# Optimization experiments

Hardware: AMD Instinct MI355X
Metric: run time of the kernel (lower is better)

Reference implementation:

```python
import jax, jax.numpy as jnp
import numpy as np

B, N = 2, 2000
C_IN, RH, RW = 256, 7, 7
D_FLAT = C_IN * RH * RW  # 12544
D_OUT = 1024
NUM_CLASSES = 10


def setup_inputs() -> dict:
    key = jax.random.key(0)
    ks = jax.random.split(key, 10)
    s1 = 1.0 / np.sqrt(D_FLAT)
    s2 = 1.0 / np.sqrt(D_OUT)
    return {
        "features": jax.random.normal(ks[0], (B, N, C_IN, RH, RW), jnp.float32),
        "boxes": jax.random.normal(ks[1], (B, N, 5), jnp.float32),
        "w1": jax.random.uniform(ks[2], (D_FLAT, D_OUT), jnp.float32, -s1, s1),
        "b1": jax.random.uniform(ks[3], (D_OUT,), jnp.float32, -s1, s1),
        "w2": jax.random.uniform(ks[4], (D_OUT, D_OUT), jnp.float32, -s2, s2),
        "b2": jax.random.uniform(ks[5], (D_OUT,), jnp.float32, -s2, s2),
        "wc": jax.random.uniform(ks[6], (D_OUT, NUM_CLASSES + 1), jnp.float32, -s2, s2),
        "bc": jax.random.uniform(ks[7], (NUM_CLASSES + 1,), jnp.float32, -s2, s2),
        "wr": jax.random.uniform(ks[8], (D_OUT, 5), jnp.float32, -s2, s2),
        "br": jax.random.uniform(ks[9], (5,), jnp.float32, -s2, s2),
    }


def reference(features, boxes, w1, b1, w2, b2, wc, bc, wr, br):
    # Flatten(start_dim=2): [B, N, C*7*7]
    x = features.reshape(B, N, D_FLAT)
    # fc: Linear -> ReLU -> Linear -> ReLU
    h = jax.nn.relu(jnp.einsum("bnd,de->bne", x, w1) + b1)
    h = jax.nn.relu(jnp.einsum("bnd,de->bne", h, w2) + b2)
    classification = jnp.einsum("bnd,dc->bnc", h, wc) + bc  # [B, N, num_classes+1]
    regression = jnp.einsum("bnd,dr->bnr", h, wr) + br      # [B, N, 5]
    boxes_out = boxes + regression
    rois = boxes
    return classification, boxes_out, rois
```

## Files before the change

kernel.cpp:

```cpp
#include <hip/hip_runtime.h>
#include <stdint.h>

#define GAS __attribute__((address_space(1)))
#define LAS __attribute__((address_space(3)))

typedef short bf16x8 __attribute__((ext_vector_type(8)));
typedef float f32x4 __attribute__((ext_vector_type(4)));
typedef unsigned short u16x8 __attribute__((ext_vector_type(8)));

__device__ __forceinline__ unsigned short f2bf(float f) {
  union { float f; uint32_t u; } v; v.f = f;
  uint32_t r = v.u + 0x7FFFu + ((v.u >> 16) & 1u);
  return (unsigned short)(r >> 16);
}

__global__ __launch_bounds__(256) void cvt_kernel(const float* __restrict__ src,
                                                  unsigned short* __restrict__ dst,
                                                  long n8) {
  long i = (long)blockIdx.x * blockDim.x + threadIdx.x;
  if (i >= n8) return;
  const float4* s4 = (const float4*)src;
  float4 a = s4[i * 2];
  float4 b = s4[i * 2 + 1];
  u16x8 o;
  o[0] = f2bf(a.x); o[1] = f2bf(a.y); o[2] = f2bf(a.z); o[3] = f2bf(a.w);
  o[4] = f2bf(b.x); o[5] = f2bf(b.y); o[6] = f2bf(b.z); o[7] = f2bf(b.w);
  ((u16x8*)dst)[i] = o;
}

__global__ __launch_bounds__(256) void transpose_cvt(const float* __restrict__ src,
                                                     unsigned short* __restrict__ dst,
                                                     int R, int C) {
  __shared__ unsigned short tile[32][33];
  int tx = threadIdx.x, ty = threadIdx.y;
  int r0 = blockIdx.y * 32, c0 = blockIdx.x * 32;
#pragma unroll
  for (int i = 0; i < 32; i += 8)
    tile[ty + i][tx] = f2bf(src[(long)(r0 + ty + i) * C + c0 + tx]);
  __syncthreads();
#pragma unroll
  for (int i = 0; i < 32; i += 8)
    dst[(long)(c0 + ty + i) * R + r0 + tx] = tile[tx][ty + i];
}

__global__ __launch_bounds__(256) void bias_relu_cvt(const float* __restrict__ acc,
                                                     const float* __restrict__ bias,
                                                     unsigned short* __restrict__ dst) {
  long i = (long)blockIdx.x * 256 + threadIdx.x;
  const float4* a4 = (const float4*)acc;
  float4 a = a4[i * 2];
  float4 b = a4[i * 2 + 1];
  int col = (int)((i * 8) & 1023);
  const float4* b4 = (const float4*)(bias + col);
  float4 ba = b4[0], bb = b4[1];
  u16x8 o;
  o[0] = f2bf(fmaxf(a.x + ba.x, 0.f)); o[1] = f2bf(fmaxf(a.y + ba.y, 0.f));
  o[2] = f2bf(fmaxf(a.z + ba.z, 0.f)); o[3] = f2bf(fmaxf(a.w + ba.w, 0.f));
  o[4] = f2bf(fmaxf(b.x + bb.x, 0.f)); o[5] = f2bf(fmaxf(b.y + bb.y, 0.f));
  o[6] = f2bf(fmaxf(b.z + bb.z, 0.f)); o[7] = f2bf(fmaxf(b.w + bb.w, 0.f));
  ((u16x8*)dst)[i] = o;
}

template <int ATOMIC, int STORE_BF16>
__global__ __launch_bounds__(256, 2) void gemm_bt(const unsigned short* __restrict__ A,
                                                  const unsigned short* __restrict__ Bt,
                                                  const float* __restrict__ bias,
                                                  void* __restrict__ Cv, int M, int K,
                                                  int kIters) {
  __shared__ unsigned short lA[128 * 64];
  __shared__ unsigned short lB[128 * 64];
  const int tid = threadIdx.x;
  const int lane = tid & 63;
  const int wave = tid >> 6;
  const int wm = wave >> 1, wn = wave & 1;
  const long rowBase = (long)blockIdx.y * 128;
  const long colBase = (long)blockIdx.x * 128;
  const int kStart = blockIdx.z * kIters * 64;

  f32x4 acc[4][4];
#pragma unroll
  for (int i = 0; i < 4; i++)
#pragma unroll
    for (int j = 0; j < 4; j++) acc[i][j] = (f32x4){0.f, 0.f, 0.f, 0.f};

  long gA[4], gB[4];
#pragma unroll
  for (int it = 0; it < 4; ++it) {
    int f = it * 256 + tid;
    int r = f >> 3;
    int q = f & 7;
    int kq = ((q ^ (r & 7)) * 8) + kStart;
    long ar = rowBase + r;
    if (ar >= M) ar = M - 1;
    gA[it] = ar * (long)K + kq;
    gB[it] = (colBase + r) * (long)K + kq;
  }

  for (int ki = 0; ki < kIters; ++ki) {
    const long kc = (long)ki * 64;
#pragma unroll
    for (int it = 0; it < 4; ++it) {
      int f = it * 256 + tid;
      __builtin_amdgcn_global_load_lds((const GAS void*)(A + gA[it] + kc),
                                       (LAS void*)(lA + f * 8), 16, 0, 0);
    }
#pragma unroll
    for (int it = 0; it < 4; ++it) {
      int f = it * 256 + tid;
      __builtin_amdgcn_global_load_lds((const GAS void*)(Bt + gB[it] + kc),
                                       (LAS void*)(lB + f * 8), 16, 0, 0);
    }
    __syncthreads();
#pragma unroll
    for (int ks = 0; ks < 64; ks += 32) {
      bf16x8 af[4], bf[4];
      const int c = (ks >> 3) + (lane >> 4);
      const int slot = (c ^ (lane & 7)) << 3;
      const int mr = wm * 64 + (lane & 15);
      const int nr = wn * 64 + (lane & 15);
#pragma unroll
      for (int i = 0; i < 4; i++)
        af[i] = *(const bf16x8*)(lA + (mr + i * 16) * 64 + slot);
#pragma unroll
      for (int i = 0; i < 4; i++)
        bf[i] = *(const bf16x8*)(lB + (nr + i * 16) * 64 + slot);
#pragma unroll
      for (int i = 0; i < 4; i++)
#pragma unroll
        for (int j = 0; j < 4; j++)
          acc[i][j] = __builtin_amdgcn_mfma_f32_16x16x32_bf16(af[i], bf[j], acc[i][j], 0, 0, 0);
    }
    __syncthreads();
  }

  const int cq = lane & 15;
  const int rq = (lane >> 4) * 4;
#pragma unroll
  for (int i = 0; i < 4; i++) {
#pragma unroll
    for (int j = 0; j < 4; j++) {
      int col = (int)colBase + wn * 64 + j * 16 + cq;
      float bv = ATOMIC ? 0.f : bias[col];
#pragma unroll
      for (int r = 0; r < 4; r++) {
        long grow = rowBase + wm * 64 + i * 16 + rq + r;
        if (grow < M) {
          if (ATOMIC) {
            unsafeAtomicAdd(&((float*)Cv)[grow * 1024 + col], acc[i][j][r]);
          } else {
            float v = acc[i][j][r] + bv;
            v = v > 0.f ? v : 0.f;
            if (STORE_BF16)
              ((unsigned short*)Cv)[grow * 1024 + col] = f2bf(v);
            else
              ((float*)Cv)[grow * 1024 + col] = v;
          }
        }
      }
    }
  }
}

__global__ __launch_bounds__(256) void head_kernel(
    const float* __restrict__ H2, const float* __restrict__ wc, const float* __restrict__ bc,
    const float* __restrict__ wr, const float* __restrict__ br, const float* __restrict__ boxes,
    float* __restrict__ cls, float* __restrict__ bout, float* __restrict__ rois) {
  const int lane = threadIdx.x & 63;
  const int wave = threadIdx.x >> 6;
  const int row = blockIdx.x * 4 + wave;
  const float* h = H2 + (long)row * 1024;
  float acc[16];
#pragma unroll
  for (int c = 0; c < 16; c++) acc[c] = 0.f;
#pragma unroll
  for (int i = 0; i < 16; i++) {
    int d = i * 64 + lane;
    float hv = h[d];
#pragma unroll
    for (int c = 0; c < 11; c++) acc[c] += hv * wc[d * 11 + c];
#pragma unroll
    for (int c = 0; c < 5; c++) acc[11 + c] += hv * wr[d * 5 + c];
  }
#pragma unroll
  for (int off = 32; off >= 1; off >>= 1) {
#pragma unroll
    for (int c = 0; c < 16; c++) acc[c] += __shfl_down(acc[c], off);
  }
  if (lane == 0) {
#pragma unroll
    for (int c = 0; c < 11; c++) cls[row * 11 + c] = acc[c] + bc[c];
#pragma unroll
    for (int c = 0; c < 5; c++) {
      float rg = acc[11 + c] + br[c];
      float bx = boxes[row * 5 + c];
      bout[row * 5 + c] = bx + rg;
      rois[row * 5 + c] = bx;
    }
  }
}

extern "C" void kernel_launch(void* const* d_in, const int* in_sizes, int n_in,
                              void* d_out, int out_size, void* d_ws, size_t ws_size,
                              hipStream_t stream) {
  const float* features = (const float*)d_in[0];
  const float* boxes = (const float*)d_in[1];
  const float* w1 = (const float*)d_in[2];
  const float* b1 = (const float*)d_in[3];
  const float* w2 = (const float*)d_in[4];
  const float* b2 = (const float*)d_in[5];
  const float* wc = (const float*)d_in[6];
  const float* bc = (const float*)d_in[7];
  const float* wr = (const float*)d_in[8];
  const float* br = (const float*)d_in[9];

  char* ws = (char*)d_ws;
  unsigned short* Xb  = (unsigned short*)ws;
  unsigned short* W1T = (unsigned short*)(ws + 100352000);
  unsigned short* W2T = (unsigned short*)(ws + 126042112);
  unsigned short* H1  = (unsigned short*)(ws + 128139264);
  float*          H2  = (float*)(ws + 136331264);
  float*          H1f = H2;

  hipMemsetAsync(H1f, 0, 16384000, stream);
  {
    long n8 = 50176000 / 8;
    cvt_kernel<<<(int)(n8 / 256), 256, 0, stream>>>(features, Xb, n8);
  }
  transpose_cvt<<<dim3(32, 392), dim3(32, 8), 0, stream>>>(w1, W1T, 12544, 1024);
  transpose_cvt<<<dim3(32, 32), dim3(32, 8), 0, stream>>>(w2, W2T, 1024, 1024);
  gemm_bt<1, 0><<<dim3(8, 32, 4), 256, 0, stream>>>(Xb, W1T, b1, H1f, 4000, 12544, 49);
  bias_relu_cvt<<<2000, 256, 0, stream>>>(H1f, b1, H1);
  gemm_bt<0, 0><<<dim3(8, 32, 1), 256, 0, stream>>>(H1, W2T, b2, H2, 4000, 1024, 16);
  float* cls = (float*)d_out;
  float* bout = cls + 44000;
  float* rois = cls + 64000;
  head_kernel<<<1000, 256, 0, stream>>>(H2, wc, bc, wr, br, boxes, cls, bout, rois);
}
```

Before: 546.5 us.

## Fuse fp32-to-bf16 conversion into GEMM1 A-load, split-K GEMM2, XCD-aware block mapping

Removes the separate feature conversion pass: GEMM1 now reads fp32 features directly, truncates them to bf16 with byte-permutes, and writes them to LDS, which drops a full read/write pass over the 200MB input. GEMM2 becomes split-K with atomic accumulation across 4 partitions, with bias and ReLU moved into the head kernel. Blocks are launched on a 1D grid remapped so that neighbouring tiles share an XCD for L2 reuse. The costs are register-staged loads in place of direct-to-LDS loads, truncation instead of round-to-nearest for the features, a larger memset, and extra atomics in GEMM2.

```diff
diff --git a/kernel.cpp b/kernel.cpp
--- a/kernel.cpp
+++ b/kernel.cpp
@@ -12,20 +12,6 @@
   union { float f; uint32_t u; } v; v.f = f;
   uint32_t r = v.u + 0x7FFFu + ((v.u >> 16) & 1u);
   return (unsigned short)(r >> 16);
-}
-
-__global__ __launch_bounds__(256) void cvt_kernel(const float* __restrict__ src,
-                                                  unsigned short* __restrict__ dst,
-                                                  long n8) {
-  long i = (long)blockIdx.x * blockDim.x + threadIdx.x;
-  if (i >= n8) return;
-  const float4* s4 = (const float4*)src;
-  float4 a = s4[i * 2];
-  float4 b = s4[i * 2 + 1];
-  u16x8 o;
-  o[0] = f2bf(a.x); o[1] = f2bf(a.y); o[2] = f2bf(a.z); o[3] = f2bf(a.w);
-  o[4] = f2bf(b.x); o[5] = f2bf(b.y); o[6] = f2bf(b.z); o[7] = f2bf(b.w);
-  ((u16x8*)dst)[i] = o;
 }
 
 __global__ __launch_bounds__(256) void transpose_cvt(const float* __restrict__ src,
@@ -61,11 +47,10 @@
   ((u16x8*)dst)[i] = o;
 }
 
-template <int ATOMIC, int STORE_BF16>
-__global__ __launch_bounds__(256, 2) void gemm_bt(const unsigned short* __restrict__ A,
+template <int A_FP32>
+__global__ __launch_bounds__(256, 2) void gemm_bt(const void* __restrict__ Av,
                                                   const unsigned short* __restrict__ Bt,
-                                                  const float* __restrict__ bias,
-                                                  void* __restrict__ Cv, int M, int K,
+                                                  float* __restrict__ Cv, int M, int K,
                                                   int kIters) {
   __shared__ unsigned short lA[128 * 64];
   __shared__ unsigned short lB[128 * 64];
@@ -73,9 +58,18 @@
   const int lane = tid & 63;
   const int wave = tid >> 6;
   const int wm = wave >> 1, wn = wave & 1;
-  const long rowBase = (long)blockIdx.y * 128;
-  const long colBase = (long)blockIdx.x * 128;
-  const int kStart = blockIdx.z * kIters * 64;
+
+  const int b = blockIdx.x;
+  const int xcd = b & 7;
+  const int slot = b >> 3;
+  const int bx = slot & 7;
+  const int pg = xcd * 16 + (slot >> 3);
+  const int by = pg & 31;
+  const int bz = pg >> 5;
+
+  const long rowBase = (long)by * 128;
+  const long colBase = (long)bx * 128;
+  const int kStart = bz * kIters * 64;
 
   f32x4 acc[4][4];
 #pragma unroll
@@ -93,16 +87,39 @@
     long ar = rowBase + r;
     if (ar >= M) ar = M - 1;
     gA[it] = ar * (long)K + kq;
-    gB[it] = (colBase + r) * (long)K + kq;
+    gB[it] = ((long)(colBase + r)) * K + kq;
   }
 
   for (int ki = 0; ki < kIters; ++ki) {
     const long kc = (long)ki * 64;
-#pragma unroll
-    for (int it = 0; it < 4; ++it) {
-      int f = it * 256 + tid;
-      __builtin_amdgcn_global_load_lds((const GAS void*)(A + gA[it] + kc),
-                                       (LAS void*)(lA + f * 8), 16, 0, 0);
+    if (A_FP32) {
+      const uint4* A4 = (const uint4*)Av;
+      uint4 t[8];
+#pragma unroll
+      for (int it = 0; it < 4; ++it) {
+        long fi = (gA[it] + kc) >> 2;
+        t[2 * it] = A4[fi];
+        t[2 * it + 1] = A4[fi + 1];
+      }
+#pragma unroll
+      for (int it = 0; it < 4; ++it) {
+        int f = it * 256 + tid;
+        uint4 lo = t[2 * it], hi = t[2 * it + 1];
+        uint4 o;
+        o.x = __builtin_amdgcn_perm(lo.y, lo.x, 0x07060302u);
+        o.y = __builtin_amdgcn_perm(lo.w, lo.z, 0x07060302u);
+        o.z = __builtin_amdgcn_perm(hi.y, hi.x, 0x07060302u);
+        o.w = __builtin_amdgcn_perm(hi.w, hi.z, 0x07060302u);
+        *(uint4*)(lA + f * 8) = o;
+      }
+    } else {
+      const unsigned short* A = (const unsigned short*)Av;
+#pragma unroll
+      for (int it = 0; it < 4; ++it) {
+        int f = it * 256 + tid;
+        __builtin_amdgcn_global_load_lds((const GAS void*)(A + gA[it] + kc),
+                                         (LAS void*)(lA + f * 8), 16, 0, 0);
+      }
     }
 #pragma unroll
     for (int it = 0; it < 4; ++it) {
@@ -115,15 +132,15 @@
     for (int ks = 0; ks < 64; ks += 32) {
       bf16x8 af[4], bf[4];
       const int c = (ks >> 3) + (lane >> 4);
-      const int slot = (c ^ (lane & 7)) << 3;
+      const int slotk = (c ^ (lane & 7)) << 3;
       const int mr = wm * 64 + (lane & 15);
       const int nr = wn * 64 + (lane & 15);
 #pragma unroll
       for (int i = 0; i < 4; i++)
-        af[i] = *(const bf16x8*)(lA + (mr + i * 16) * 64 + slot);
+        af[i] = *(const bf16x8*)(lA + (mr + i * 16) * 64 + slotk);
 #pragma unroll
       for (int i = 0; i < 4; i++)
-        bf[i] = *(const bf16x8*)(lB + (nr + i * 16) * 64 + slot);
+        bf[i] = *(const bf16x8*)(lB + (nr + i * 16) * 64 + slotk);
 #pragma unroll
       for (int i = 0; i < 4; i++)
 #pragma unroll
@@ -140,42 +157,32 @@
 #pragma unroll
     for (int j = 0; j < 4; j++) {
       int col = (int)colBase + wn * 64 + j * 16 + cq;
-      float bv = ATOMIC ? 0.f : bias[col];
 #pragma unroll
       for (int r = 0; r < 4; r++) {
         long grow = rowBase + wm * 64 + i * 16 + rq + r;
-        if (grow < M) {
-          if (ATOMIC) {
-            unsafeAtomicAdd(&((float*)Cv)[grow * 1024 + col], acc[i][j][r]);
-          } else {
-            float v = acc[i][j][r] + bv;
-            v = v > 0.f ? v : 0.f;
-            if (STORE_BF16)
-              ((unsigned short*)Cv)[grow * 1024 + col] = f2bf(v);
-            else
-              ((float*)Cv)[grow * 1024 + col] = v;
-          }
-        }
+        if (grow < M) unsafeAtomicAdd(&Cv[grow * 1024 + col], acc[i][j][r]);
       }
     }
   }
 }
 
 __global__ __launch_bounds__(256) void head_kernel(
-    const float* __restrict__ H2, const float* __restrict__ wc, const float* __restrict__ bc,
-    const float* __restrict__ wr, const float* __restrict__ br, const float* __restrict__ boxes,
+    const float* __restrict__ H2f, const float* __restrict__ b2,
+    const float* __restrict__ wc, const float* __restrict__ bc,
+    const float* __restrict__ wr, const float* __restrict__ br,
+    const float* __restrict__ boxes,
     float* __restrict__ cls, float* __restrict__ bout, float* __restrict__ rois) {
   const int lane = threadIdx.x & 63;
   const int wave = threadIdx.x >> 6;
   const int row = blockIdx.x * 4 + wave;
-  const float* h = H2 + (long)row * 1024;
+  const float* h = H2f + (long)row * 1024;
   float acc[16];
 #pragma unroll
   for (int c = 0; c < 16; c++) acc[c] = 0.f;
 #pragma unroll
   for (int i = 0; i < 16; i++) {
     int d = i * 64 + lane;
-    float hv = h[d];
+    float hv = fmaxf(h[d] + b2[d], 0.f);
 #pragma unroll
     for (int c = 0; c < 11; c++) acc[c] += hv * wc[d * 11 + c];
 #pragma unroll
@@ -214,25 +221,20 @@
   const float* br = (const float*)d_in[9];
 
   char* ws = (char*)d_ws;
-  unsigned short* Xb  = (unsigned short*)ws;
-  unsigned short* W1T = (unsigned short*)(ws + 100352000);
-  unsigned short* W2T = (unsigned short*)(ws + 126042112);
-  unsigned short* H1  = (unsigned short*)(ws + 128139264);
-  float*          H2  = (float*)(ws + 136331264);
-  float*          H1f = H2;
-
-  hipMemsetAsync(H1f, 0, 16384000, stream);
-  {
-    long n8 = 50176000 / 8;
-    cvt_kernel<<<(int)(n8 / 256), 256, 0, stream>>>(features, Xb, n8);
-  }
+  unsigned short* W1T = (unsigned short*)ws;
+  unsigned short* W2T = (unsigned short*)(ws + 25690112);
+  unsigned short* H1  = (unsigned short*)(ws + 27787264);
+  float*          H1f = (float*)(ws + 35979264);
+  float*          H2f = (float*)(ws + 52363264);
+
+  hipMemsetAsync(H1f, 0, 32768000, stream);
   transpose_cvt<<<dim3(32, 392), dim3(32, 8), 0, stream>>>(w1, W1T, 12544, 1024);
   transpose_cvt<<<dim3(32, 32), dim3(32, 8), 0, stream>>>(w2, W2T, 1024, 1024);
-  gemm_bt<1, 0><<<dim3(8, 32, 4), 256, 0, stream>>>(Xb, W1T, b1, H1f, 4000, 12544, 49);
+  gemm_bt<1><<<1024, 256, 0, stream>>>(features, W1T, H1f, 4000, 12544, 49);
   bias_relu_cvt<<<2000, 256, 0, stream>>>(H1f, b1, H1);
-  gemm_bt<0, 0><<<dim3(8, 32, 1), 256, 0, stream>>>(H1, W2T, b2, H2, 4000, 1024, 16);
+  gemm_bt<0><<<1024, 256, 0, stream>>>(H1, W2T, H2f, 4000, 1024, 4);
   float* cls = (float*)d_out;
   float* bout = cls + 44000;
   float* rois = cls + 64000;
-  head_kernel<<<1000, 256, 0, stream>>>(H2, wc, bc, wr, br, boxes, cls, bout, rois);
-}
+  head_kernel<<<1000, 256, 0, stream>>>(H2f, b2, wc, bc, wr, br, boxes, cls, bout, rois);
+}
```

New measurement: 561.8 us. 1.03x slower.
